# Kernel optimization log

Hardware: AMD Instinct MI355X
Metric: run time of the kernel (lower is better)

The kernel has to match this reference:

```python
import jax, jax.numpy as jnp
import numpy as np
from math import comb

# Module hyperparameters (init_kwargs)
B_, C_, H_, W_, M_, N_ = 256, 3, 256, 256, 31, 31


def _bernstein(num_samples: int, deg: int) -> np.ndarray:
    """Bernstein basis evaluated at pixel-center points t_i=(i+0.5)/num_samples.
    Returns (num_samples, deg+1): C(deg,k) * t^k * (1-t)^(deg-k)."""
    t = (np.arange(num_samples, dtype=np.float64) + 0.5) / num_samples
    k = np.arange(deg + 1)
    coeff = np.array([comb(deg, i) for i in range(deg + 1)], dtype=np.float64)
    basis = coeff * (t[:, None] ** k) * ((1.0 - t[:, None]) ** (deg - k))
    return basis.astype(np.float32)


def _bez_basis() -> np.ndarray:
    # Full separable basis, matching bez_filter: (H, W, M+1, N+1)
    bu = _bernstein(H_, M_)  # (H, M+1)
    bv = _bernstein(W_, N_)  # (W, N+1)
    return bu[:, None, :, None] * bv[None, :, None, :]


_BASIS = jnp.asarray(_bez_basis())  # (H, W, M+1, N+1) constant, not trainable


def setup_inputs() -> dict:
    key = jax.random.key(0)
    K_mat = jax.random.normal(key, (B_, C_, M_ + 1, N_ + 1), dtype=jnp.float32) * 0.05
    x = jnp.zeros((1,), dtype=jnp.int32)  # `inputs` is ignored by the layer
    return {"x": x, "K_mat": K_mat}


def reference(x, K_mat):
    # out[b,c,i,j] = sum_{p,q} K_mat[b,c,p,q] * basis[i,j,p,q]
    # Single batched GEMM replacing b*c tiny conv2d launches.
    out = jnp.einsum('bcpq,hwpq->bchw', K_mat, _BASIS)
    return out[None]  # (1, b, c, h, w) per compute_output_shape
```

## Files before the change

kernel.cpp:

```cpp
#include <hip/hip_runtime.h>


#define DEG 31

typedef short bf16x8 __attribute__((ext_vector_type(8)));
typedef float f32x4  __attribute__((ext_vector_type(4)));

__device__ __forceinline__ unsigned short f2bf_rne(float x) {
    unsigned int u = __float_as_uint(x);
    unsigned int r = (u + 0x7FFFu + ((u >> 16) & 1u)) >> 16;
    return (unsigned short)r;
}
__device__ __forceinline__ float bf2f(unsigned short h) {
    return __uint_as_float(((unsigned int)h) << 16);
}

__global__ __launch_bounds__(256) void bez_basis_kernel(
        float* __restrict__ Bt,
        unsigned short* __restrict__ Hi,
        unsigned short* __restrict__ Lo) {
    int g = blockIdx.x * 256 + threadIdx.x;
    int i = g >> 5;
    int k = g & 31;
    double t = ((double)i + 0.5) / 256.0;
    double coeff = 1.0;
    for (int kk = 1; kk <= k; ++kk)
        coeff = coeff * (double)(DEG - kk + 1) / (double)kk;
    double tk = 1.0;
    for (int e = 0; e < k; ++e) tk *= t;
    double omt = 1.0 - t;
    double tq = 1.0;
    for (int e = 0; e < DEG - k; ++e) tq *= omt;
    float v = (float)(coeff * tk * tq);
    Bt[g] = v;
    unsigned short h = f2bf_rne(v);
    Hi[g] = h;
    Lo[g] = f2bf_rne(v - bf2f(h));
}

__global__ __launch_bounds__(256) void bez_main_kernel(
        const float* __restrict__ K,
        const float* __restrict__ Bt,
        const unsigned short* __restrict__ Hi,
        const unsigned short* __restrict__ Lo,
        float* __restrict__ out) {
    __shared__ __align__(16) unsigned short sThi[256 * 32];
    __shared__ __align__(16) unsigned short sTlo[256 * 32];

    const int bc   = blockIdx.x;
    const int tid  = threadIdx.x;
    const int lane = tid & 63;
    const int w    = tid >> 6;

    float breg[32];
    const float4* brow = (const float4*)(Bt + tid * 32);
    #pragma unroll
    for (int q4 = 0; q4 < 8; ++q4) {
        float4 v = brow[q4];
        breg[q4 * 4 + 0] = v.x;
        breg[q4 * 4 + 1] = v.y;
        breg[q4 * 4 + 2] = v.z;
        breg[q4 * 4 + 3] = v.w;
    }
    const float* Kbc = K + (size_t)bc * 1024;
    float treg[32];
    #pragma unroll
    for (int p = 0; p < 32; ++p) {
        float acc = 0.0f;
        #pragma unroll
        for (int q = 0; q < 32; ++q)
            acc += Kbc[p * 32 + q] * breg[q];
        treg[p] = acc;
    }
    const int jsw = (tid >> 1) & 3;
    #pragma unroll
    for (int c = 0; c < 4; ++c) {
        bf16x8 vh, vl;
        #pragma unroll
        for (int jj = 0; jj < 8; ++jj) {
            float x = treg[c * 8 + jj];
            unsigned short h = f2bf_rne(x);
            vh[jj] = (short)h;
            vl[jj] = (short)f2bf_rne(x - bf2f(h));
        }
        int off = tid * 32 + (c ^ jsw) * 8;
        *(bf16x8*)&sThi[off] = vh;
        *(bf16x8*)&sTlo[off] = vl;
    }
    __syncthreads();

    const int m = lane & 15;
    const int q = lane >> 4;

    bf16x8 Th[4], Tl[4];
    #pragma unroll
    for (int a = 0; a < 4; ++a) {
        int j = (w * 4 + a) * 16 + m;
        int off = j * 32 + (q ^ ((j >> 1) & 3)) * 8;
        Th[a] = *(const bf16x8*)&sThi[off];
        Tl[a] = *(const bf16x8*)&sTlo[off];
    }

    float* outbc = out + (size_t)bc * 65536;
    for (int it = 0; it < 16; ++it) {
        int i = it * 16 + m;
        bf16x8 Bh = *(const bf16x8*)(Hi + i * 32 + q * 8);
        bf16x8 Bl = *(const bf16x8*)(Lo + i * 32 + q * 8);
        #pragma unroll
        for (int a = 0; a < 4; ++a) {
            f32x4 acc = {0.0f, 0.0f, 0.0f, 0.0f};
            acc = __builtin_amdgcn_mfma_f32_16x16x32_bf16(Tl[a], Bh, acc, 0, 0, 0);
            acc = __builtin_amdgcn_mfma_f32_16x16x32_bf16(Th[a], Bl, acc, 0, 0, 0);
            acc = __builtin_amdgcn_mfma_f32_16x16x32_bf16(Th[a], Bh, acc, 0, 0, 0);
            float4 o4 = {acc[0], acc[1], acc[2], acc[3]};
            float* o = outbc + (size_t)i * 256 + (w * 4 + a) * 16 + q * 4;
            *(float4*)o = o4;
        }
    }
}

extern "C" void kernel_launch(void* const* d_in, const int* in_sizes, int n_in,
                              void* d_out, int out_size, void* d_ws, size_t ws_size,
                              hipStream_t stream) {
    const float* K = (const float*)d_in[1];
    char* ws = (char*)d_ws;
    float*          Bt = (float*)ws;
    unsigned short* Hi = (unsigned short*)(ws + 32768);
    unsigned short* Lo = (unsigned short*)(ws + 49152);
    float* out = (float*)d_out;

    bez_basis_kernel<<<dim3(32), dim3(256), 0, stream>>>(Bt, Hi, Lo);
    bez_main_kernel<<<dim3(768), dim3(256), 0, stream>>>(K, Bt, Hi, Lo, out);
}
```

Measured before the change: 215.1 us.

## Fuse Bernstein basis generation into main kernel and stage basis in LDS

Removes the separate basis-generation kernel. Each block now computes its own Bernstein row with a double-precision recurrence and writes the hi/lo bf16 split into swizzled shared memory. The MFMA loop then reads the basis from LDS instead of global memory. This saves one launch and the global basis traffic, but every block repeats the fp64 basis computation and LDS use doubles to 64KB, which may lower occupancy.

```diff
diff --git a/kernel.cpp b/kernel.cpp
--- a/kernel.cpp
+++ b/kernel.cpp
@@ -15,73 +15,65 @@
     return __uint_as_float(((unsigned int)h) << 16);
 }
 
-__global__ __launch_bounds__(256) void bez_basis_kernel(
-        float* __restrict__ Bt,
-        unsigned short* __restrict__ Hi,
-        unsigned short* __restrict__ Lo) {
-    int g = blockIdx.x * 256 + threadIdx.x;
-    int i = g >> 5;
-    int k = g & 31;
-    double t = ((double)i + 0.5) / 256.0;
-    double coeff = 1.0;
-    for (int kk = 1; kk <= k; ++kk)
-        coeff = coeff * (double)(DEG - kk + 1) / (double)kk;
-    double tk = 1.0;
-    for (int e = 0; e < k; ++e) tk *= t;
-    double omt = 1.0 - t;
-    double tq = 1.0;
-    for (int e = 0; e < DEG - k; ++e) tq *= omt;
-    float v = (float)(coeff * tk * tq);
-    Bt[g] = v;
-    unsigned short h = f2bf_rne(v);
-    Hi[g] = h;
-    Lo[g] = f2bf_rne(v - bf2f(h));
-}
-
-__global__ __launch_bounds__(256) void bez_main_kernel(
+__global__ __launch_bounds__(256) void bez_fused_kernel(
         const float* __restrict__ K,
-        const float* __restrict__ Bt,
-        const unsigned short* __restrict__ Hi,
-        const unsigned short* __restrict__ Lo,
         float* __restrict__ out) {
     __shared__ __align__(16) unsigned short sThi[256 * 32];
     __shared__ __align__(16) unsigned short sTlo[256 * 32];
+    __shared__ __align__(16) unsigned short sBhi[256 * 32];
+    __shared__ __align__(16) unsigned short sBlo[256 * 32];
 
     const int bc   = blockIdx.x;
     const int tid  = threadIdx.x;
     const int lane = tid & 63;
     const int w    = tid >> 6;
+    const int jsw  = (tid >> 1) & 3;
 
+    double t   = ((double)tid + 0.5) * (1.0 / 256.0);
+    double omt = 1.0 - t;
+    double r   = t / omt;
+    double o2 = omt * omt, o4 = o2 * o2, o8 = o4 * o4, o16 = o8 * o8;
+    double b  = o16 * o8 * o4 * o2 * omt;
     float breg[32];
-    const float4* brow = (const float4*)(Bt + tid * 32);
     #pragma unroll
-    for (int q4 = 0; q4 < 8; ++q4) {
-        float4 v = brow[q4];
-        breg[q4 * 4 + 0] = v.x;
-        breg[q4 * 4 + 1] = v.y;
-        breg[q4 * 4 + 2] = v.z;
-        breg[q4 * 4 + 3] = v.w;
+    for (int k = 0; k < 32; ++k) {
+        breg[k] = (float)b;
+        b *= ((double)(DEG - k) / (double)(k + 1)) * r;
     }
+    #pragma unroll
+    for (int c = 0; c < 4; ++c) {
+        bf16x8 vh, vl;
+        #pragma unroll
+        for (int e = 0; e < 8; ++e) {
+            float x = breg[c * 8 + e];
+            unsigned short h = f2bf_rne(x);
+            vh[e] = (short)h;
+            vl[e] = (short)f2bf_rne(x - bf2f(h));
+        }
+        int off = tid * 32 + (c ^ jsw) * 8;
+        *(bf16x8*)&sBhi[off] = vh;
+        *(bf16x8*)&sBlo[off] = vl;
+    }
+
     const float* Kbc = K + (size_t)bc * 1024;
     float treg[32];
     #pragma unroll
     for (int p = 0; p < 32; ++p) {
         float acc = 0.0f;
         #pragma unroll
-        for (int q = 0; q < 32; ++q)
-            acc += Kbc[p * 32 + q] * breg[q];
+        for (int qi = 0; qi < 32; ++qi)
+            acc += Kbc[p * 32 + qi] * breg[qi];
         treg[p] = acc;
     }
-    const int jsw = (tid >> 1) & 3;
     #pragma unroll
     for (int c = 0; c < 4; ++c) {
         bf16x8 vh, vl;
         #pragma unroll
-        for (int jj = 0; jj < 8; ++jj) {
-            float x = treg[c * 8 + jj];
+        for (int e = 0; e < 8; ++e) {
+            float x = treg[c * 8 + e];
             unsigned short h = f2bf_rne(x);
-            vh[jj] = (short)h;
-            vl[jj] = (short)f2bf_rne(x - bf2f(h));
+            vh[e] = (short)h;
+            vl[e] = (short)f2bf_rne(x - bf2f(h));
         }
         int off = tid * 32 + (c ^ jsw) * 8;
         *(bf16x8*)&sThi[off] = vh;
@@ -104,8 +96,9 @@
     float* outbc = out + (size_t)bc * 65536;
     for (int it = 0; it < 16; ++it) {
         int i = it * 16 + m;
-        bf16x8 Bh = *(const bf16x8*)(Hi + i * 32 + q * 8);
-        bf16x8 Bl = *(const bf16x8*)(Lo + i * 32 + q * 8);
+        int boff = i * 32 + (q ^ ((i >> 1) & 3)) * 8;
+        bf16x8 Bh = *(const bf16x8*)&sBhi[boff];
+        bf16x8 Bl = *(const bf16x8*)&sBlo[boff];
         #pragma unroll
         for (int a = 0; a < 4; ++a) {
             f32x4 acc = {0.0f, 0.0f, 0.0f, 0.0f};
@@ -123,12 +116,7 @@
                               void* d_out, int out_size, void* d_ws, size_t ws_size,
                               hipStream_t stream) {
     const float* K = (const float*)d_in[1];
-    char* ws = (char*)d_ws;
-    float*          Bt = (float*)ws;
-    unsigned short* Hi = (unsigned short*)(ws + 32768);
-    unsigned short* Lo = (unsigned short*)(ws + 49152);
     float* out = (float*)d_out;
-
-    bez_basis_kernel<<<dim3(32), dim3(256), 0, stream>>>(Bt, Hi, Lo);
-    bez_main_kernel<<<dim3(768), dim3(256), 0, stream>>>(K, Bt, Hi, Lo, out);
+    (void)d_ws; (void)ws_size;
+    bez_fused_kernel<<<dim3(768), dim3(256), 0, stream>>>(K, out);
 }
```

Result: slower. 222.1 us (+3.3%).
